# Optimization experiments

Measured on AMD Instinct MI355X. Metric: run time of the kernel, lower is better.

Reference implementation:

```python
import jax, jax.numpy as jnp
import numpy as np
from jax import lax

NUM_EMBEDDING = 512
D_EMBEDDING = 256
COMMITMENT_COST = 0.25
B = 131072


def setup_inputs() -> dict:
    key = jax.random.key(0)
    k1, k2, k3 = jax.random.split(key, 3)
    node_type = jax.random.randint(k1, (B,), 0, 10, dtype=jnp.int64 if jax.config.jax_enable_x64 else jnp.int32)
    node_representation = jax.random.normal(k2, (B, D_EMBEDDING), dtype=jnp.float32)
    # nn.Embedding default init: N(0, 1)
    codebook = jax.random.normal(k3, (NUM_EMBEDDING, D_EMBEDDING), dtype=jnp.float32)
    return {"node_type": node_type, "node_representation": node_representation, "codebook": codebook}


def _code_indices(node_type, z, codebook):
    # Map atom type -> codebook quadrant: C(5)->0, N(6)->1, O(7)->2, others->3
    K = codebook.shape[0]
    qsize = K // 4
    group = jnp.where(node_type == 5, 0,
            jnp.where(node_type == 6, 1,
            jnp.where(node_type == 7, 2, 3)))  # [b]
    # Squared L2 distances to all codes: ||z||^2 + ||e||^2 - 2 z.e  -> [b, K]
    d2 = (jnp.sum(z * z, axis=1, keepdims=True)
          + jnp.sum(codebook * codebook, axis=1)
          - 2.0 * (z @ codebook.T))
    col_group = jnp.arange(K) // qsize  # [K], quadrant of each code
    valid = group[:, None] == col_group[None, :]  # [b, K]
    # Masked argmin == per-quadrant argmin (+ quadrant offset), as in the original.
    return jnp.argmin(jnp.where(valid, d2, jnp.inf), axis=1)


def reference(node_type, node_representation, codebook):
    z = node_representation
    idx = _code_indices(node_type, z, codebook)          # [b]
    quantized = codebook[idx]                            # [b, d]
    vq_loss = jnp.mean((quantized - lax.stop_gradient(z)) ** 2)
    commitment_loss = COMMITMENT_COST * jnp.mean((z - lax.stop_gradient(quantized)) ** 2)
    # Straight-through estimator
    quantized_st = z + lax.stop_gradient(quantized - z)
    return (vq_loss, commitment_loss, idx, quantized_st)
```

## Files before the change

### kernel.cpp

```cpp
#include <hip/hip_runtime.h>


#define B_ROWS   131072
#define D_EMB    256
#define TPB      256
#define SGRID    1025
#define THETA    0.0625f

#define WS_WSUM   0
#define WS_GCNT   516
#define WS_GPOSD  532
#define WS_CBH    1024
#define WS_CBL    (WS_CBH + 262144)
#define WS_EN     (WS_CBL + 262144)
#define WS_ROWS   (WS_EN + 2048)
#define WS_NEED   (WS_ROWS + 524288)
#define WS_FLAGS  8

typedef __attribute__((ext_vector_type(8))) short bf16x8;
typedef __attribute__((ext_vector_type(4))) float f32x4;

__device__ __forceinline__ float bf2f(unsigned short u) {
    return __uint_as_float(((unsigned)u) << 16);
}

__device__ __forceinline__ void splitA(const float4& a0, const float4& a1,
                                       bf16x8& ah, bf16x8& al) {
    float ff[8] = {a0.x, a0.y, a0.z, a0.w, a1.x, a1.y, a1.z, a1.w};
    #pragma unroll
    for (int j = 0; j < 8; ++j) {
        unsigned u = __float_as_uint(ff[j]);
        ah[j] = (short)(u >> 16);
        float r = ff[j] - __uint_as_float(u & 0xffff0000u);
        al[j] = (short)(__float_as_uint(r) >> 16);
    }
}

__global__ void vq_prep2(const float* __restrict__ cbf, const int* __restrict__ nt,
                         unsigned short* __restrict__ cbh, unsigned short* __restrict__ cbl,
                         float* __restrict__ eN, int* __restrict__ gcnt) {
    __shared__ int sI64, c4[4];
    const int bid = blockIdx.x;
    const int tid = threadIdx.x;

    if (tid < 4) c4[tid] = 0;

    if (tid < 64) {
        const int lane = tid;
        float4 v = *(const float4*)(cbf + bid * 256 + lane * 4);
        unsigned u0 = __float_as_uint(v.x), u1 = __float_as_uint(v.y);
        unsigned u2 = __float_as_uint(v.z), u3 = __float_as_uint(v.w);
        ushort4 h = make_ushort4((unsigned short)(u0 >> 16), (unsigned short)(u1 >> 16),
                                 (unsigned short)(u2 >> 16), (unsigned short)(u3 >> 16));
        float r0 = v.x - __uint_as_float(u0 & 0xffff0000u);
        float r1 = v.y - __uint_as_float(u1 & 0xffff0000u);
        float r2 = v.z - __uint_as_float(u2 & 0xffff0000u);
        float r3 = v.w - __uint_as_float(u3 & 0xffff0000u);
        ushort4 l = make_ushort4((unsigned short)(__float_as_uint(r0) >> 16),
                                 (unsigned short)(__float_as_uint(r1) >> 16),
                                 (unsigned short)(__float_as_uint(r2) >> 16),
                                 (unsigned short)(__float_as_uint(r3) >> 16));
        *(ushort4*)(cbh + bid * 256 + lane * 4) = h;
        *(ushort4*)(cbl + bid * 256 + lane * 4) = l;
        float s = fmaf(v.x, v.x, fmaf(v.y, v.y, fmaf(v.z, v.z, v.w * v.w)));
        #pragma unroll
        for (int d = 1; d < 64; d <<= 1) s += __shfl_xor(s, d);
        if (lane == 0) eN[bid] = s;
    } else if (tid < 128) {
        int o = (nt[2 * (tid - 64) + 1] != 0) ? 1 : 0;
        unsigned long long m = __ballot(o != 0);
        if (tid == 64) sI64 = (m == 0ULL) ? 1 : 0;
    }
    __syncthreads();

    const int i64 = sI64;
    const int row = bid * 256 + tid;
    const int tv  = i64 ? nt[2 * row] : nt[row];
    const int g   = (tv == 5) ? 0 : (tv == 6) ? 1 : (tv == 7) ? 2 : 3;
    atomicAdd(&c4[g], 1);
    __syncthreads();
    if (tid < 4) atomicAdd(&gcnt[tid], c4[tid]);
}

__global__ void vq_binoff(const int* __restrict__ nt, const int* __restrict__ gcnt,
                          int* __restrict__ gposD, int* __restrict__ rows) {
    __shared__ int sI64, basev[4], pos[4];
    const int tid = threadIdx.x;
    if (tid < 4) pos[tid] = 0;
    if (tid >= 64 && tid < 128) {
        int o = (nt[2 * (tid - 64) + 1] != 0) ? 1 : 0;
        unsigned long long m = __ballot(o != 0);
        if (tid == 64) sI64 = (m == 0ULL) ? 1 : 0;
    }
    __syncthreads();
    const int i64 = sI64;
    const int row = blockIdx.x * 256 + tid;
    const int tv  = i64 ? nt[2 * row] : nt[row];
    const int g   = (tv == 5) ? 0 : (tv == 6) ? 1 : (tv == 7) ? 2 : 3;
    atomicAdd(&pos[g], 1);
    __syncthreads();
    if (tid < 4) {
        int c0 = gcnt[0], c1 = gcnt[1], c2 = gcnt[2];
        int off = (tid == 0) ? 0 : (tid == 1) ? c0 : (tid == 2) ? (c0 + c1) : (c0 + c1 + c2);
        basev[tid] = off + atomicAdd(&gposD[tid], pos[tid]);
        pos[tid] = 0;
    }
    __syncthreads();
    int p = atomicAdd(&pos[g], 1);
    rows[basev[g] + p] = row;
}

__global__ __launch_bounds__(TPB, 3) void vq_score6(
    const float* __restrict__ zf,
    const float* __restrict__ cbf,
    const unsigned short* __restrict__ cbh,
    const unsigned short* __restrict__ cbl,
    const float* __restrict__ eN,
    const int* __restrict__ rows,
    const int* __restrict__ gcnt,
    float* __restrict__ out,
    double* __restrict__ wsum)
{
    __shared__ int2   sT[4][16];
    __shared__ float2 sM[4][16];
    __shared__ float  sZZ[4][16];
    __shared__ int    sW[4][32];
    __shared__ double sRed[4];

    const int tid  = threadIdx.x;
    const int wave = tid >> 6;
    const int lane = tid & 63;
    const int col  = lane & 15;
    const int quad = lane >> 4;
    const int w    = blockIdx.x * 4 + wave;

    const int cnt0 = gcnt[0], cnt1 = gcnt[1], cnt2 = gcnt[2], cnt3 = gcnt[3];
    const int off1 = cnt0, off2 = off1 + cnt1, off3 = off2 + cnt2;
    const int tl0 = (cnt0 + 31) >> 5, tl1 = (cnt1 + 31) >> 5, tl2 = (cnt2 + 31) >> 5;
    const int tl3 = (cnt3 + 31) >> 5;
    const int to1 = tl0, to2 = to1 + tl1, to3 = to2 + tl2, tot = to3 + tl3;

    double lacc = 0.0;

    if (w < tot) {
        int g, b, offg, cntg;
        if (w < to1)      { g = 0; b = w;       offg = 0;    cntg = cnt0; }
        else if (w < to2) { g = 1; b = w - to1; offg = off1; cntg = cnt1; }
        else if (w < to3) { g = 2; b = w - to2; offg = off2; cntg = cnt2; }
        else              { g = 3; b = w - to3; offg = off3; cntg = cnt3; }
        const int base = offg + b * 32;
        int nr = cntg - b * 32; if (nr > 32) nr = 32;
        const int nr0  = (nr < 16) ? nr : 16;
        const int nr1  = nr - 16;

        int ix0 = base + ((col < nr0) ? col : (nr0 - 1));
        int ix1 = (nr1 > 0) ? (base + 16 + ((col < nr1) ? col : (nr1 - 1))) : ix0;
        const float* za0 = zf + rows[ix0] * 256 + quad * 8;
        const float* za1 = zf + rows[ix1] * 256 + quad * 8;
        const unsigned short* bhp = cbh + (g * 128 + col) * 256 + quad * 8;
        const unsigned short* blp = cbl + (g * 128 + col) * 256 + quad * 8;

        f32x4 acc[2][8];
        #pragma unroll
        for (int st = 0; st < 2; ++st)
            #pragma unroll
            for (int t = 0; t < 8; ++t) acc[st][t] = (f32x4){0.f, 0.f, 0.f, 0.f};
        float zz0 = 0.f, zz1 = 0.f;

        #pragma unroll
        for (int c = 0; c < 8; ++c) {
            float4 a00 = *(const float4*)(za0 + c * 32);
            float4 a01 = *(const float4*)(za0 + c * 32 + 4);
            float4 a10 = *(const float4*)(za1 + c * 32);
            float4 a11 = *(const float4*)(za1 + c * 32 + 4);
            zz0 = fmaf(a00.x,a00.x,fmaf(a00.y,a00.y,fmaf(a00.z,a00.z,fmaf(a00.w,a00.w,zz0))));
            zz0 = fmaf(a01.x,a01.x,fmaf(a01.y,a01.y,fmaf(a01.z,a01.z,fmaf(a01.w,a01.w,zz0))));
            zz1 = fmaf(a10.x,a10.x,fmaf(a10.y,a10.y,fmaf(a10.z,a10.z,fmaf(a10.w,a10.w,zz1))));
            zz1 = fmaf(a11.x,a11.x,fmaf(a11.y,a11.y,fmaf(a11.z,a11.z,fmaf(a11.w,a11.w,zz1))));
            bf16x8 ah0, al0, ah1, al1;
            splitA(a00, a01, ah0, al0);
            splitA(a10, a11, ah1, al1);
            #pragma unroll
            for (int t = 0; t < 8; ++t) {
                bf16x8 bh = *(const bf16x8*)(bhp + t * 4096 + c * 32);
                bf16x8 bl = *(const bf16x8*)(blp + t * 4096 + c * 32);
                acc[0][t] = __builtin_amdgcn_mfma_f32_16x16x32_bf16(ah0, bh, acc[0][t], 0, 0, 0);
                acc[0][t] = __builtin_amdgcn_mfma_f32_16x16x32_bf16(al0, bh, acc[0][t], 0, 0, 0);
                acc[0][t] = __builtin_amdgcn_mfma_f32_16x16x32_bf16(ah0, bl, acc[0][t], 0, 0, 0);
                acc[1][t] = __builtin_amdgcn_mfma_f32_16x16x32_bf16(ah1, bh, acc[1][t], 0, 0, 0);
                acc[1][t] = __builtin_amdgcn_mfma_f32_16x16x32_bf16(al1, bh, acc[1][t], 0, 0, 0);
                acc[1][t] = __builtin_amdgcn_mfma_f32_16x16x32_bf16(ah1, bl, acc[1][t], 0, 0, 0);
            }
        }
        zz0 += __shfl_xor(zz0, 16); zz0 += __shfl_xor(zz0, 32);
        zz1 += __shfl_xor(zz1, 16); zz1 += __shfl_xor(zz1, 32);

        float e8[8];
        #pragma unroll
        for (int t = 0; t < 8; ++t) e8[t] = eN[g * 128 + t * 16 + col];

        for (int st = 0; st < 2; ++st) {
            const int nrs = st ? nr1 : nr0;
            if (nrs <= 0) continue;
            if (quad == 0) sZZ[wave][col] = st ? zz1 : zz0;

            #pragma unroll
            for (int r = 0; r < 4; ++r) {
                float m1 = __builtin_inff(), m2 = __builtin_inff();
                int   i1 = 0x7fffffff,      i2 = 0x7fffffff;
                #pragma unroll
                for (int t = 0; t < 8; ++t) {
                    float sc = e8[t] - 2.f * acc[st][t][r];
                    int   ci = t * 16 + col;
                    if (sc < m1 || (sc == m1 && ci < i1)) { m2 = m1; i2 = i1; m1 = sc; i1 = ci; }
                    else if (sc < m2 || (sc == m2 && ci < i2)) { m2 = sc; i2 = ci; }
                }
                #pragma unroll
                for (int d2 = 1; d2 < 16; d2 <<= 1) {
                    float b1 = __shfl_xor(m1, d2);
                    int  bi1 = __shfl_xor(i1, d2);
                    float b2 = __shfl_xor(m2, d2);
                    int  bi2 = __shfl_xor(i2, d2);
                    if (b1 < m1 || (b1 == m1 && bi1 < i1)) {
                        float om = m1; int oi = i1;
                        m1 = b1; i1 = bi1;
                        if (b2 < om || (b2 == om && bi2 < oi)) { m2 = b2; i2 = bi2; }
                        else                                   { m2 = om; i2 = oi; }
                    } else {
                        if (b1 < m2 || (b1 == m2 && bi1 < i2)) { m2 = b1; i2 = bi1; }
                    }
                }
                if (col == 0) {
                    sT[wave][quad * 4 + r] = make_int2(i1, i2);
                    sM[wave][quad * 4 + r] = make_float2(m1, m2);
                }
            }

            const int s  = lane >> 2;
            const int pq = lane & 3;
            const bool valid = (s < nrs);
            int grow = 0, c1 = 0, c2 = 0;
            float scm1 = 0.f, scm2 = 1e30f, zzr = 0.f;
            if (valid) {
                grow = rows[base + st * 16 + s];
                int2  tt = sT[wave][s];
                float2 mm = sM[wave][s];
                zzr = sZZ[wave][s];
                c1 = g * 128 + tt.x;
                c2 = g * 128 + tt.y;
                scm1 = mm.x; scm2 = mm.y;
            }
            int    wfin  = c1;
            double dfull = (double)(zzr + scm1);
            const bool need = valid && (scm2 - scm1 <= THETA);

            if (__any(need)) {
                double d1c = 0.0, d2c = 0.0;
                if (need) {
                    const float* zp = zf  + grow * 256 + pq * 64;
                    const float* p1 = cbf + c1 * 256 + pq * 64;
                    const float* p2 = cbf + c2 * 256 + pq * 64;
                    #pragma unroll 4
                    for (int it = 0; it < 16; ++it) {
                        float4 fz = *(const float4*)(zp + it * 4);
                        float4 g1 = *(const float4*)(p1 + it * 4);
                        float4 g2 = *(const float4*)(p2 + it * 4);
                        double e;
                        e = (double)fz.x - (double)g1.x; d1c = fma(e, e, d1c);
                        e = (double)fz.y - (double)g1.y; d1c = fma(e, e, d1c);
                        e = (double)fz.z - (double)g1.z; d1c = fma(e, e, d1c);
                        e = (double)fz.w - (double)g1.w; d1c = fma(e, e, d1c);
                        e = (double)fz.x - (double)g2.x; d2c = fma(e, e, d2c);
                        e = (double)fz.y - (double)g2.y; d2c = fma(e, e, d2c);
                        e = (double)fz.z - (double)g2.z; d2c = fma(e, e, d2c);
                        e = (double)fz.w - (double)g2.w; d2c = fma(e, e, d2c);
                    }
                }
                double t1 = d1c + __shfl_xor(d1c, 1); t1 += __shfl_xor(t1, 2);
                double t2 = d2c + __shfl_xor(d2c, 1); t2 += __shfl_xor(t2, 2);
                if (need) {
                    bool take1 = (t1 < t2) || (t1 == t2 && c1 < c2);
                    wfin  = take1 ? c1 : c2;
                    dfull = take1 ? t1 : t2;
                }
            }

            if (valid && pq == 0) {
                lacc += dfull;
                sW[wave][st * 16 + s] = wfin;
                out[2 + grow] = (float)wfin;
            }
        }

        for (int r = 0; r < nr; ++r) {
            const int wv = sW[wave][r];
            const int gr2 = rows[base + r];
            const float4 v = *(const float4*)(cbf + wv * 256 + lane * 4);
            const int ob = 2 + B_ROWS + gr2 * 256;
            *(float2*)(out + ob + lane * 4)     = make_float2(v.x, v.y);
            *(float2*)(out + ob + lane * 4 + 2) = make_float2(v.z, v.w);
        }
    }

    #pragma unroll
    for (int d2 = 1; d2 < 64; d2 <<= 1) lacc += __shfl_xor(lacc, d2);
    if (lane == 0) sRed[wave] = lacc;
    __syncthreads();
    if (tid == 0) atomicAdd(&wsum[blockIdx.x & 63], sRed[0] + sRed[1] + sRed[2] + sRed[3]);
}

__global__ void vq_detect(const unsigned short* cb, const int* nt, int* flag) {
    __shared__ int cnt, odd;
    if (threadIdx.x == 0) { cnt = 0; odd = 0; }
    __syncthreads();
    int c = 0, o = 0;
    for (int i = threadIdx.x; i < 512; i += 64) {
        unsigned short u = cb[2 * i];
        int e = (u >> 7) & 0xFF;
        if (e < 100 || e > 140) c++;
    }
    if (nt[2 * threadIdx.x + 1] != 0) o = 1;
    atomicAdd(&cnt, c);
    atomicAdd(&odd, o);
    __syncthreads();
    if (threadIdx.x == 0) {
        flag[0] = (cnt < 50) ? 1 : 0;
        flag[1] = (odd == 0) ? 1 : 0;
    }
}

__global__ __launch_bounds__(512, 2) void vq_main_f32(
    const int* __restrict__ nt,
    const float* __restrict__ zff,
    const float* __restrict__ cbf,
    float* __restrict__ out,
    double* __restrict__ wsum,
    const int* __restrict__ flag)
{
    if (flag[0] != 0) return;
    const int i64 = flag[1];

    __shared__ float  sE[256 * 132];
    __shared__ float  sZ[128 * 32];
    __shared__ int    sList[512];
    __shared__ int    sCnt[4], sPos[4];
    __shared__ int    sTop1[128], sTop2[128];
    __shared__ float  sEe[128];
    __shared__ double sRed[8];

    const int tid  = threadIdx.x;
    const int row0 = blockIdx.x * 512;

    if (tid < 4) { sCnt[tid] = 0; sPos[tid] = 0; }
    __syncthreads();
    {
        int t = i64 ? nt[2 * (row0 + tid)] : nt[row0 + tid];
        int g = (t == 5) ? 0 : (t == 6) ? 1 : (t == 7) ? 2 : 3;
        atomicAdd(&sCnt[g], 1);
        __syncthreads();
        int o1 = sCnt[0], o2 = o1 + sCnt[1], o3 = o2 + sCnt[2];
        int offg = (g == 0) ? 0 : (g == 1) ? o1 : (g == 2) ? o2 : o3;
        int p = atomicAdd(&sPos[g], 1);
        sList[offg + p] = row0 + tid;
    }
    __syncthreads();

    int cnt[4], off[4];
    cnt[0] = sCnt[0]; cnt[1] = sCnt[1]; cnt[2] = sCnt[2]; cnt[3] = sCnt[3];
    off[0] = 0; off[1] = cnt[0]; off[2] = off[1] + cnt[1]; off[3] = off[2] + cnt[2];

    const int ccol = tid & 31, rrow = tid >> 5;
    const int c0 = ccol * 4, rbase = rrow * 8;
    double lacc = 0.0;

    for (int gg = 0; gg < 4; ++gg) {
        const int n = cnt[gg];
        if (n == 0) continue;
        __syncthreads();
        for (int i = tid; i < 128 * 256; i += 512) {
            int c = i >> 8, k = i & 255;
            sE[k * 132 + c] = cbf[(gg * 128 + c) * 256 + k];
        }
        __syncthreads();
        if (tid < 128) {
            float s = 0.f;
            for (int k = 0; k < 256; ++k) { float v = sE[k * 132 + tid]; s = fmaf(v, v, s); }
            sEe[tid] = s;
        }
        __syncthreads();

        const int ntiles = (n + 127) >> 7;
        for (int tI = 0; tI < ntiles; ++tI) {
            const int tbase = off[gg] + tI * 128;
            const int nrows = min(128, n - tI * 128);
            float acc[8][4];
            #pragma unroll
            for (int r = 0; r < 8; ++r)
                #pragma unroll
                for (int q = 0; q < 4; ++q) acc[r][q] = 0.f;

            for (int kb = 0; kb < 8; ++kb) {
                __syncthreads();
                #pragma unroll
                for (int it = 0; it < 2; ++it) {
                    int i = it * 512 + tid;
                    int s = i >> 3, j = i & 7;
                    float4 v = make_float4(0.f, 0.f, 0.f, 0.f);
                    if (s < nrows) {
                        int gr = sList[tbase + s];
                        v = *(const float4*)(zff + gr * 256 + kb * 32 + j * 4);
                    }
                    *(float4*)&sZ[s * 32 + j * 4] = v;
                }
                __syncthreads();
                #pragma unroll
                for (int k4 = 0; k4 < 8; ++k4) {
                    const int kk = kb * 32 + k4 * 4;
                    const float4 e0 = *(const float4*)&sE[(kk + 0) * 132 + c0];
                    const float4 e1 = *(const float4*)&sE[(kk + 1) * 132 + c0];
                    const float4 e2 = *(const float4*)&sE[(kk + 2) * 132 + c0];
                    const float4 e3 = *(const float4*)&sE[(kk + 3) * 132 + c0];
                    #pragma unroll
                    for (int r = 0; r < 8; ++r) {
                        const float4 zv = *(const float4*)&sZ[(rbase + r) * 32 + k4 * 4];
                        acc[r][0] = fmaf(zv.x, e0.x, fmaf(zv.y, e1.x, fmaf(zv.z, e2.x, fmaf(zv.w, e3.x, acc[r][0]))));
                        acc[r][1] = fmaf(zv.x, e0.y, fmaf(zv.y, e1.y, fmaf(zv.z, e2.y, fmaf(zv.w, e3.y, acc[r][1]))));
                        acc[r][2] = fmaf(zv.x, e0.z, fmaf(zv.y, e1.z, fmaf(zv.z, e2.z, fmaf(zv.w, e3.z, acc[r][2]))));
                        acc[r][3] = fmaf(zv.x, e0.w, fmaf(zv.y, e1.w, fmaf(zv.z, e2.w, fmaf(zv.w, e3.w, acc[r][3]))));
                    }
                }
            }

            float eq[4] = { sEe[c0], sEe[c0 + 1], sEe[c0 + 2], sEe[c0 + 3] };
            for (int r = 0; r < 8; ++r) {
                float m1 = __builtin_inff(), m2 = __builtin_inff();
                int   i1 = 0x7fffffff,      i2 = 0x7fffffff;
                #pragma unroll
                for (int q = 0; q < 4; ++q) {
                    float sc = eq[q] - 2.f * acc[r][q];
                    int   ci = c0 + q;
                    if (sc < m1 || (sc == m1 && ci < i1)) { m2 = m1; i2 = i1; m1 = sc; i1 = ci; }
                    else if (sc < m2 || (sc == m2 && ci < i2)) { m2 = sc; i2 = ci; }
                }
                #pragma unroll
                for (int d = 1; d < 32; d <<= 1) {
                    float b1 = __shfl_xor(m1, d);
                    int  bi1 = __shfl_xor(i1, d);
                    float b2 = __shfl_xor(m2, d);
                    int  bi2 = __shfl_xor(i2, d);
                    if (b1 < m1 || (b1 == m1 && bi1 < i1)) {
                        float om = m1; int oi = i1;
                        m1 = b1; i1 = bi1;
                        if (b2 < om || (b2 == om && bi2 < oi)) { m2 = b2; i2 = bi2; }
                        else                                   { m2 = om; i2 = oi; }
                    } else {
                        if (b1 < m2 || (b1 == m2 && bi1 < i2)) { m2 = b1; i2 = bi1; }
                    }
                }
                if (ccol == 0) { sTop1[rbase + r] = i1; sTop2[rbase + r] = i2; }
            }
            __syncthreads();

            {
                const int s  = tid >> 2;
                const int pq = tid & 3;
                const bool valid = (s < nrows);
                double d1c = 0.0, d2c = 0.0;
                int gr = 0, c1g = 0, c2g = 0;
                if (valid) {
                    gr  = sList[tbase + s];
                    c1g = gg * 128 + sTop1[s];
                    c2g = gg * 128 + sTop2[s];
                    #pragma unroll 4
                    for (int it = 0; it < 16; ++it) {
                        float4 fz = *(const float4*)(zff + gr  * 256 + pq * 64 + it * 4);
                        float4 f1 = *(const float4*)(cbf + c1g * 256 + pq * 64 + it * 4);
                        float4 f2 = *(const float4*)(cbf + c2g * 256 + pq * 64 + it * 4);
                        double e;
                        e = (double)fz.x - (double)f1.x; d1c = fma(e, e, d1c);
                        e = (double)fz.y - (double)f1.y; d1c = fma(e, e, d1c);
                        e = (double)fz.z - (double)f1.z; d1c = fma(e, e, d1c);
                        e = (double)fz.w - (double)f1.w; d1c = fma(e, e, d1c);
                        e = (double)fz.x - (double)f2.x; d2c = fma(e, e, d2c);
                        e = (double)fz.y - (double)f2.y; d2c = fma(e, e, d2c);
                        e = (double)fz.z - (double)f2.z; d2c = fma(e, e, d2c);
                        e = (double)fz.w - (double)f2.w; d2c = fma(e, e, d2c);
                    }
                }
                double t1 = d1c + __shfl_xor(d1c, 1); t1 += __shfl_xor(t1, 2);
                double t2 = d2c + __shfl_xor(d2c, 1); t2 += __shfl_xor(t2, 2);
                if (valid) {
                    bool take1 = (t1 < t2) || (t1 == t2 && c1g < c2g);
                    int  w = take1 ? c1g : c2g;
                    lacc += take1 ? d1c : d2c;
                    const int obase = 2 + B_ROWS + gr * 256 + pq * 64;
                    #pragma unroll 4
                    for (int it = 0; it < 16; ++it) {
                        float4 f4 = *(const float4*)(cbf + w * 256 + pq * 64 + it * 4);
                        *(float2*)(out + obase + it * 4)     = make_float2(f4.x, f4.y);
                        *(float2*)(out + obase + it * 4 + 2) = make_float2(f4.z, f4.w);
                    }
                    if (pq == 0) out[2 + gr] = (float)w;
                }
            }
        }
    }

    #pragma unroll
    for (int d = 1; d < 64; d <<= 1) lacc += __shfl_xor(lacc, d);
    if ((tid & 63) == 0) sRed[tid >> 6] = lacc;
    __syncthreads();
    if (tid == 0) {
        double s = 0.0;
        #pragma unroll
        for (int i = 0; i < 8; ++i) s += sRed[i];
        atomicAdd(wsum, s);
    }
}

__global__ void vq_fin(const double* wsum, float* out, int n) {
    if (threadIdx.x == 0 && blockIdx.x == 0) {
        double m = 0.0;
        for (int i = 0; i < n; ++i) m += wsum[i];
        m /= ((double)B_ROWS * (double)D_EMB);
        out[0] = (float)m;
        out[1] = (float)(0.25 * m);
    }
}

extern "C" void kernel_launch(void* const* d_in, const int* in_sizes, int n_in,
                              void* d_out, int out_size, void* d_ws, size_t ws_size,
                              hipStream_t stream) {
    const int*   nt  = (const int*)d_in[0];
    const float* zf  = (const float*)d_in[1];
    const float* cbf = (const float*)d_in[2];
    float*  out  = (float*)d_out;
    double* wsum = (double*)((char*)d_ws + WS_WSUM);

    hipMemsetAsync(d_ws, 0, 1024, stream);

    if (ws_size >= (size_t)WS_NEED) {
        unsigned short* cbh  = (unsigned short*)((char*)d_ws + WS_CBH);
        unsigned short* cbl  = (unsigned short*)((char*)d_ws + WS_CBL);
        float* eN    = (float*)((char*)d_ws + WS_EN);
        int*   gcnt  = (int*)((char*)d_ws + WS_GCNT);
        int*   gposD = (int*)((char*)d_ws + WS_GPOSD);
        int*   rowsp = (int*)((char*)d_ws + WS_ROWS);
        vq_prep2<<<512, 256, 0, stream>>>(cbf, nt, cbh, cbl, eN, gcnt);
        vq_binoff<<<512, 256, 0, stream>>>(nt, gcnt, gposD, rowsp);
        vq_score6<<<SGRID, TPB, 0, stream>>>(zf, cbf, cbh, cbl, eN, rowsp, gcnt,
                                             out, wsum);
        vq_fin<<<1, 64, 0, stream>>>(wsum, out, 64);
    } else {
        int* flag = (int*)((char*)d_ws + WS_FLAGS);
        vq_detect<<<1, 64, 0, stream>>>((const unsigned short*)cbf, nt, flag);
        vq_main_f32<<<256, 512, 0, stream>>>(nt, zf, cbf, out, wsum, flag);
        vq_fin<<<1, 64, 0, stream>>>(wsum, out, 1);
    }
}
```

Measured before the change: 386.8 us.

## Tighten near-tie threshold with double-precision norms and prefetch codebook rows in writeout

Computes the row and codebook squared norms in double precision so the approximate distance is more accurate. This allows a much smaller tie threshold, which cuts how many rows need the exact double-precision recheck. The gather-writeout loop now stores the output row index in shared memory with the code index and prefetches the next codebook row while storing the current one. Double-precision FMAs in the main scoring loop add extra ALU work and register pressure.

Measured after the change: 400.9 us. 3.6% more time.

```diff
diff --git a/kernel.cpp b/kernel.cpp
--- a/kernel.cpp
+++ b/kernel.cpp
@@ -5,7 +5,7 @@
 #define D_EMB    256
 #define TPB      256
 #define SGRID    1025
-#define THETA    0.0625f
+#define THETA    0.002f
 
 #define WS_WSUM   0
 #define WS_GCNT   516
@@ -62,10 +62,12 @@
                                  (unsigned short)(__float_as_uint(r3) >> 16));
         *(ushort4*)(cbh + bid * 256 + lane * 4) = h;
         *(ushort4*)(cbl + bid * 256 + lane * 4) = l;
-        float s = fmaf(v.x, v.x, fmaf(v.y, v.y, fmaf(v.z, v.z, v.w * v.w)));
+        double s = fma((double)v.x, (double)v.x,
+                   fma((double)v.y, (double)v.y,
+                   fma((double)v.z, (double)v.z, (double)v.w * (double)v.w)));
         #pragma unroll
         for (int d = 1; d < 64; d <<= 1) s += __shfl_xor(s, d);
-        if (lane == 0) eN[bid] = s;
+        if (lane == 0) eN[bid] = (float)s;
     } else if (tid < 128) {
         int o = (nt[2 * (tid - 64) + 1] != 0) ? 1 : 0;
         unsigned long long m = __ballot(o != 0);
@@ -110,7 +112,7 @@
     rows[basev[g] + p] = row;
 }
 
-__global__ __launch_bounds__(TPB, 3) void vq_score6(
+__global__ __launch_bounds__(TPB, 3) void vq_score8(
     const float* __restrict__ zf,
     const float* __restrict__ cbf,
     const unsigned short* __restrict__ cbh,
@@ -124,7 +126,7 @@
     __shared__ int2   sT[4][16];
     __shared__ float2 sM[4][16];
     __shared__ float  sZZ[4][16];
-    __shared__ int    sW[4][32];
+    __shared__ int2   sW[4][32];
     __shared__ double sRed[4];
 
     const int tid  = threadIdx.x;
@@ -165,7 +167,7 @@
         for (int st = 0; st < 2; ++st)
             #pragma unroll
             for (int t = 0; t < 8; ++t) acc[st][t] = (f32x4){0.f, 0.f, 0.f, 0.f};
-        float zz0 = 0.f, zz1 = 0.f;
+        double zz0 = 0.0, zz1 = 0.0;
 
         #pragma unroll
         for (int c = 0; c < 8; ++c) {
@@ -173,10 +175,14 @@
             float4 a01 = *(const float4*)(za0 + c * 32 + 4);
             float4 a10 = *(const float4*)(za1 + c * 32);
             float4 a11 = *(const float4*)(za1 + c * 32 + 4);
-            zz0 = fmaf(a00.x,a00.x,fmaf(a00.y,a00.y,fmaf(a00.z,a00.z,fmaf(a00.w,a00.w,zz0))));
-            zz0 = fmaf(a01.x,a01.x,fmaf(a01.y,a01.y,fmaf(a01.z,a01.z,fmaf(a01.w,a01.w,zz0))));
-            zz1 = fmaf(a10.x,a10.x,fmaf(a10.y,a10.y,fmaf(a10.z,a10.z,fmaf(a10.w,a10.w,zz1))));
-            zz1 = fmaf(a11.x,a11.x,fmaf(a11.y,a11.y,fmaf(a11.z,a11.z,fmaf(a11.w,a11.w,zz1))));
+            zz0 = fma((double)a00.x, (double)a00.x, fma((double)a00.y, (double)a00.y,
+                  fma((double)a00.z, (double)a00.z, fma((double)a00.w, (double)a00.w, zz0))));
+            zz0 = fma((double)a01.x, (double)a01.x, fma((double)a01.y, (double)a01.y,
+                  fma((double)a01.z, (double)a01.z, fma((double)a01.w, (double)a01.w, zz0))));
+            zz1 = fma((double)a10.x, (double)a10.x, fma((double)a10.y, (double)a10.y,
+                  fma((double)a10.z, (double)a10.z, fma((double)a10.w, (double)a10.w, zz1))));
+            zz1 = fma((double)a11.x, (double)a11.x, fma((double)a11.y, (double)a11.y,
+                  fma((double)a11.z, (double)a11.z, fma((double)a11.w, (double)a11.w, zz1))));
             bf16x8 ah0, al0, ah1, al1;
             splitA(a00, a01, ah0, al0);
             splitA(a10, a11, ah1, al1);
@@ -202,7 +208,7 @@
         for (int st = 0; st < 2; ++st) {
             const int nrs = st ? nr1 : nr0;
             if (nrs <= 0) continue;
-            if (quad == 0) sZZ[wave][col] = st ? zz1 : zz0;
+            if (quad == 0) sZZ[wave][col] = (float)(st ? zz1 : zz0);
 
             #pragma unroll
             for (int r = 0; r < 4; ++r) {
@@ -287,18 +293,26 @@
 
             if (valid && pq == 0) {
                 lacc += dfull;
-                sW[wave][st * 16 + s] = wfin;
+                sW[wave][st * 16 + s] = make_int2(wfin, grow);
                 out[2 + grow] = (float)wfin;
             }
         }
 
-        for (int r = 0; r < nr; ++r) {
-            const int wv = sW[wave][r];
-            const int gr2 = rows[base + r];
-            const float4 v = *(const float4*)(cbf + wv * 256 + lane * 4);
-            const int ob = 2 + B_ROWS + gr2 * 256;
-            *(float2*)(out + ob + lane * 4)     = make_float2(v.x, v.y);
-            *(float2*)(out + ob + lane * 4 + 2) = make_float2(v.z, v.w);
+        {
+            int2  wg = sW[wave][0];
+            float4 v = *(const float4*)(cbf + wg.x * 256 + lane * 4);
+            for (int r = 0; r < nr; ++r) {
+                int2  nwg = wg;
+                float4 nv = v;
+                if (r + 1 < nr) {
+                    nwg = sW[wave][r + 1];
+                    nv  = *(const float4*)(cbf + nwg.x * 256 + lane * 4);
+                }
+                const int ob = 2 + B_ROWS + wg.y * 256;
+                *(float2*)(out + ob + lane * 4)     = make_float2(v.x, v.y);
+                *(float2*)(out + ob + lane * 4 + 2) = make_float2(v.z, v.w);
+                wg = nwg; v = nv;
+            }
         }
     }
 
@@ -548,7 +562,7 @@
         int*   rowsp = (int*)((char*)d_ws + WS_ROWS);
         vq_prep2<<<512, 256, 0, stream>>>(cbf, nt, cbh, cbl, eN, gcnt);
         vq_binoff<<<512, 256, 0, stream>>>(nt, gcnt, gposD, rowsp);
-        vq_score6<<<SGRID, TPB, 0, stream>>>(zf, cbf, cbh, cbl, eN, rowsp, gcnt,
+        vq_score8<<<SGRID, TPB, 0, stream>>>(zf, cbf, cbh, cbl, eN, rowsp, gcnt,
                                              out, wsum);
         vq_fin<<<1, 64, 0, stream>>>(wsum, out, 64);
     } else {
```
